# Performance work log

Hardware: AMD Instinct MI355X
Metric: run time of the kernel (lower is better)

The kernel has to match this reference:

```python
import jax, jax.numpy as jnp
import numpy as np

EMBED = 1024
FF = 4096
LN_EPS = 1e-5

def _layernorm(x, gamma, beta):
    mu = jnp.mean(x, axis=-1, keepdims=True)
    var = jnp.var(x, axis=-1, keepdims=True)
    return (x - mu) * jax.lax.rsqrt(var + LN_EPS) * gamma + beta

def setup_inputs() -> dict:
    key = jax.random.key(0)
    ks = jax.random.split(key, 16)
    s = 1.0 / np.sqrt(EMBED)
    s2 = 1.0 / np.sqrt(FF)
    return {
        "x": jax.random.normal(ks[0], (8, 2048, EMBED), dtype=jnp.float32),
        "Wq": jax.random.uniform(ks[1], (EMBED, EMBED), jnp.float32, -s, s),
        "bq": jnp.zeros((EMBED,), jnp.float32),
        "Wk": jax.random.uniform(ks[2], (EMBED, EMBED), jnp.float32, -s, s),
        "bk": jnp.zeros((EMBED,), jnp.float32),
        "Wv": jax.random.uniform(ks[3], (EMBED, EMBED), jnp.float32, -s, s),
        "bv": jnp.zeros((EMBED,), jnp.float32),
        "Wo": jax.random.uniform(ks[4], (EMBED, EMBED), jnp.float32, -s, s),
        "bo": jnp.zeros((EMBED,), jnp.float32),
        "g1": jnp.ones((EMBED,), jnp.float32),
        "b1": jnp.zeros((EMBED,), jnp.float32),
        "g2": jnp.ones((EMBED,), jnp.float32),
        "b2": jnp.zeros((EMBED,), jnp.float32),
        "W1": jax.random.uniform(ks[5], (EMBED, FF), jnp.float32, -s, s),
        "bf1": jnp.zeros((FF,), jnp.float32),
        "W2": jax.random.uniform(ks[6], (FF, EMBED), jnp.float32, -s2, s2),
        "bf2": jnp.zeros((EMBED,), jnp.float32),
    }

def reference(x, Wq, bq, Wk, bk, Wv, bv, Wo, bo, g1, b1, g2, b2, W1, bf1, W2, bf2):
    # Single-head attention (heads arg unused in original forward)
    Q = jnp.einsum('bse,ef->bsf', x, Wq) + bq
    K = jnp.einsum('bse,ef->bsf', x, Wk) + bk
    V = jnp.einsum('bse,ef->bsf', x, Wv) + bv
    scale = 1.0 / jnp.sqrt(jnp.float32(EMBED))
    scores = jnp.einsum('bqe,bke->bqk', Q, K) * scale  # [B,S,S]
    attn = jax.nn.softmax(scores, axis=-1)
    attn_out = jnp.einsum('bqk,bke->bqe', attn, V)
    attn_out = jnp.einsum('bse,ef->bsf', attn_out, Wo) + bo
    # dropout is identity in eval mode
    h = _layernorm(x + attn_out, g1, b1)
    ffn = jnp.einsum('bsf,fh->bsh', jax.nn.relu(jnp.einsum('bse,eh->bsh', h, W1) + bf1), W2) + bf2
    return _layernorm(h + ffn, g2, b2)
```

## Files before the change

kernel.cpp:

```cpp
#include <hip/hip_runtime.h>


typedef __attribute__((ext_vector_type(4))) float  f32x4;
typedef __attribute__((ext_vector_type(8))) short  s16x8;
typedef __attribute__((ext_vector_type(4))) short  s16x4;
typedef unsigned short u16;
typedef unsigned int   u32;

__device__ __forceinline__ float bf2f(short s) {
  u32 u = ((u32)(u16)s) << 16;
  float f; __builtin_memcpy(&f, &u, 4); return f;
}
__device__ __forceinline__ short f2bf(float f) {
  u32 u; __builtin_memcpy(&u, &f, 4);
  u32 r = (u + 0x7fffu + ((u >> 16) & 1u)) >> 16;
  return (short)(u16)r;
}

__device__ __forceinline__ void gload16(const void* g, void* l) {
  __builtin_amdgcn_global_load_lds(
      (const __attribute__((address_space(1))) u32*)g,
      (__attribute__((address_space(3))) u32*)l, 16, 0, 0);
}

template<int MODE>
__global__ __launch_bounds__(512, 4)
void gemm256(const u16* __restrict__ A, const u16* __restrict__ BT,
             u16* __restrict__ C,
             const float* __restrict__ bias0, const float* __restrict__ bias1,
             const float* __restrict__ bias2, const float* __restrict__ linv,
             int M, int N, int K, float scale,
             long long sA, long long sB, long long sC) {
  __shared__ u16 SMEM[24576];

  const int gx = gridDim.x, gy = gridDim.y;
  const int nwg = gx * gy * gridDim.z;
  const int orig = (blockIdx.z * gy + blockIdx.y) * gx + blockIdx.x;
  const int q = nwg >> 3, r8 = nwg & 7;
  const int xcd = orig & 7, pos = orig >> 3;
  const int wg = (xcd < r8 ? xcd * (q + 1) : r8 * (q + 1) + (xcd - r8) * q) + pos;
  const int bz = wg / (gx * gy);
  const int rem = wg % (gx * gy);
  const long long bm = (long long)(rem / gx) * 256;
  const long long bn = (long long)(rem % gx) * 128;

  const char* Ag = (const char*)(A + (long long)bz * sA);
  const char* Bg = (const char*)(BT + (long long)bz * sB);
  u16* Cb = C + (long long)bz * sC;
  const long long ldb = (long long)K * 2;

  const int tid = threadIdx.x;
  const int lane = tid & 63, wid = tid >> 6;
  const int lr = lane & 15, kg = lane >> 4;
  const int wm = wid >> 1, wn = wid & 1;
  const int NT = K >> 5;

  f32x4 acc[4][4] = {};

  const int oA0 = tid * 16, oA1 = (512 + tid) * 16, oB0 = tid * 16;
  const long long arow0 = bm + (oA0 >> 6), arow1 = bm + (oA1 >> 6);
  const long long brow0 = bn + (oB0 >> 6);
  const int akoff0 = oA0 & 63, akoff1 = oA1 & 63, bkoff0 = oB0 & 63;

#define STAGE(TT, CN) do { \
    char* sa_ = (char*)(SMEM + (CN) * 8192); \
    char* sb_ = (char*)(SMEM + 16384 + (CN) * 4096); \
    const long long kb_ = (long long)(TT) * 64; \
    gload16(Ag + arow0 * ldb + kb_ + akoff0, sa_ + oA0); \
    gload16(Ag + arow1 * ldb + kb_ + akoff1, sa_ + oA1); \
    gload16(Bg + brow0 * ldb + kb_ + bkoff0, sb_ + oB0); \
  } while (0)

  STAGE(0, 0);
  __syncthreads();

  for (int T = 0; T < NT; ++T) {
    const int c = T & 1, cn = c ^ 1;
    if (T + 1 < NT) STAGE(T + 1, cn);

    const char* pa = (const char*)(SMEM + c * 8192);
    const char* pb = (const char*)(SMEM + 16384 + c * 4096);
    s16x8 af[4], bfr[4];
#pragma unroll
    for (int mi = 0; mi < 4; ++mi)
      af[mi] = *(const s16x8*)(pa + ((wm * 64 + mi * 16 + lr) << 6) + (kg << 4));
#pragma unroll
    for (int nj = 0; nj < 4; ++nj)
      bfr[nj] = *(const s16x8*)(pb + ((wn * 64 + nj * 16 + lr) << 6) + (kg << 4));

    __builtin_amdgcn_s_setprio(1);
#pragma unroll
    for (int mi = 0; mi < 4; ++mi)
#pragma unroll
      for (int nj = 0; nj < 4; ++nj)
        acc[mi][nj] = __builtin_amdgcn_mfma_f32_16x16x32_bf16(af[mi], bfr[nj], acc[mi][nj], 0, 0, 0);
    __builtin_amdgcn_s_setprio(0);
    __syncthreads();
  }

  const long long zM = (long long)bz * M;
  u16* obase; long long ldc, bnl;
  const float* bptr = bias0;
  if (MODE == 5) {
    const int sel = (int)(bn >> 10);
    obase = C + (long long)sel * 16777216;
    ldc = 1024; bnl = bn & 1023;
    bptr = (sel == 0 ? bias0 : sel == 1 ? bias1 : bias2);
  } else { obase = Cb; ldc = N; bnl = bn; }

#pragma unroll
  for (int b = 0; b < 2; ++b) {
    if ((wm >> 1) == b) {
      const int rbase = (wm & 1) * 64;
#pragma unroll
      for (int nj = 0; nj < 4; ++nj) {
        const int col = wn * 64 + nj * 16 + lr;
        float bv = 0.f;
        if (MODE == 1 || MODE == 2 || MODE == 5) bv = bptr[bnl + col];
#pragma unroll
        for (int mi = 0; mi < 4; ++mi) {
          const int r0 = rbase + mi * 16 + kg * 4;
#pragma unroll
          for (int r = 0; r < 4; ++r) {
            float v = acc[mi][nj][r];
            if (MODE == 1 || MODE == 2 || MODE == 5) v = v * scale + bv;
            if (MODE == 2) v = fmaxf(v, 0.f);
            if (MODE == 3) v = __expf(v * scale);
            if (MODE == 4) v = v * linv[zM + bm + b * 128 + r0 + r];
            SMEM[(r0 + r) * 128 + (col ^ (kg << 4))] = (u16)f2bf(v);
          }
        }
      }
    }
    __syncthreads();
#pragma unroll
    for (int i = 0; i < 4; ++i) {
      const int o   = (i * 512 + tid) * 16;
      const int row = o >> 8;
      const int wb  = o & 255;
      const int gs  = (wb >> 4) ^ ((((row) >> 2) & 3) << 1);
      s16x8 d = *(const s16x8*)((const char*)SMEM + row * 256 + (gs << 4));
      *(s16x8*)((char*)obase + (((long long)bm + b * 128 + row) * ldc + bnl) * 2 + wb) = d;
    }
    __syncthreads();
  }
#undef STAGE
}

__global__ __launch_bounds__(256) void cast_f32_bf16(const float* __restrict__ in,
                                                     u16* __restrict__ out) {
  long long i = (long long)blockIdx.x * 256 + threadIdx.x;
  f32x4 v = ((const f32x4*)in)[i];
  s16x4 o;
#pragma unroll
  for (int j = 0; j < 4; j++) o[j] = f2bf(v[j]);
  ((s16x4*)out)[i] = o;
}

__global__ __launch_bounds__(256) void transpose_f32_bf16(const float* __restrict__ in,
                                                          u16* __restrict__ out,
                                                          int R, int C) {
  __shared__ float tile[32][33];
  const int tx = threadIdx.x, ty = threadIdx.y;
  const int r0 = blockIdx.y * 32, c0 = blockIdx.x * 32;
#pragma unroll
  for (int i = 0; i < 32; i += 8)
    tile[ty + i][tx] = in[(long long)(r0 + ty + i) * C + (c0 + tx)];
  __syncthreads();
#pragma unroll
  for (int i = 0; i < 32; i += 8)
    out[(long long)(c0 + ty + i) * R + (r0 + tx)] = (u16)f2bf(tile[tx][ty + i]);
}

__global__ __launch_bounds__(256) void transpose_bf16_bf16(const u16* __restrict__ in,
                                                           u16* __restrict__ out,
                                                           int R, int C,
                                                           long long isb, long long osb) {
  __shared__ u16 tile[32][33];
  in  += (long long)blockIdx.z * isb;
  out += (long long)blockIdx.z * osb;
  const int tx = threadIdx.x, ty = threadIdx.y;
  const int r0 = blockIdx.y * 32, c0 = blockIdx.x * 32;
#pragma unroll
  for (int i = 0; i < 32; i += 8)
    tile[ty + i][tx] = in[(long long)(r0 + ty + i) * C + (c0 + tx)];
  __syncthreads();
#pragma unroll
  for (int i = 0; i < 32; i += 8)
    out[(long long)(c0 + ty + i) * R + (r0 + tx)] = tile[tx][ty + i];
}

__global__ __launch_bounds__(256) void rowinv2048(const u16* __restrict__ P,
                                                  float* __restrict__ linv) {
  const long long row = blockIdx.x;
  const u16* p = P + row * 2048;
  const int t = threadIdx.x;
  s16x8 raw = *(const s16x8*)&p[t * 8];
  float s = 0.f;
#pragma unroll
  for (int j = 0; j < 8; j++) s += bf2f(raw[j]);
#pragma unroll
  for (int off = 32; off > 0; off >>= 1) s += __shfl_xor(s, off);
  __shared__ float red[4];
  if ((t & 63) == 0) red[t >> 6] = s;
  __syncthreads();
  if (t == 0) {
    s = (red[0] + red[1]) + (red[2] + red[3]);
    linv[row] = 1.0f / s;
  }
}

__global__ __launch_bounds__(256) void ln_add_f32bf16(const float* __restrict__ x,
                                                      const u16* __restrict__ a,
                                                      const float* __restrict__ g,
                                                      const float* __restrict__ be,
                                                      u16* __restrict__ out) {
  const long long row = blockIdx.x;
  const int t = threadIdx.x;
  f32x4 xv = ((const f32x4*)(x + row * 1024))[t];
  s16x4 av = ((const s16x4*)(a + row * 1024))[t];
  float v[4]; float sum = 0.f, ss = 0.f;
#pragma unroll
  for (int j = 0; j < 4; j++) { v[j] = xv[j] + bf2f(av[j]); sum += v[j]; ss += v[j] * v[j]; }
#pragma unroll
  for (int off = 32; off > 0; off >>= 1) { sum += __shfl_xor(sum, off); ss += __shfl_xor(ss, off); }
  __shared__ float red[8];
  if ((t & 63) == 0) { red[t >> 6] = sum; red[4 + (t >> 6)] = ss; }
  __syncthreads();
  sum = (red[0] + red[1]) + (red[2] + red[3]);
  ss  = (red[4] + red[5]) + (red[6] + red[7]);
  const float mu   = sum * (1.f / 1024.f);
  const float var  = ss * (1.f / 1024.f) - mu * mu;
  const float rstd = rsqrtf(var + 1e-5f);
  s16x4 o;
#pragma unroll
  for (int j = 0; j < 4; j++) {
    const int c = t * 4 + j;
    o[j] = f2bf((v[j] - mu) * rstd * g[c] + be[c]);
  }
  *(s16x4*)&out[row * 1024 + t * 4] = o;
}

__global__ __launch_bounds__(256) void ln_add_bf16bf16(const u16* __restrict__ h,
                                                       const u16* __restrict__ f,
                                                       const float* __restrict__ g,
                                                       const float* __restrict__ be,
                                                       float* __restrict__ out) {
  const long long row = blockIdx.x;
  const int t = threadIdx.x;
  s16x4 hv = ((const s16x4*)(h + row * 1024))[t];
  s16x4 fv = ((const s16x4*)(f + row * 1024))[t];
  float v[4]; float sum = 0.f, ss = 0.f;
#pragma unroll
  for (int j = 0; j < 4; j++) { v[j] = bf2f(hv[j]) + bf2f(fv[j]); sum += v[j]; ss += v[j] * v[j]; }
#pragma unroll
  for (int off = 32; off > 0; off >>= 1) { sum += __shfl_xor(sum, off); ss += __shfl_xor(ss, off); }
  __shared__ float red[8];
  if ((t & 63) == 0) { red[t >> 6] = sum; red[4 + (t >> 6)] = ss; }
  __syncthreads();
  sum = (red[0] + red[1]) + (red[2] + red[3]);
  ss  = (red[4] + red[5]) + (red[6] + red[7]);
  const float mu   = sum * (1.f / 1024.f);
  const float var  = ss * (1.f / 1024.f) - mu * mu;
  const float rstd = rsqrtf(var + 1e-5f);
  f32x4 o;
#pragma unroll
  for (int j = 0; j < 4; j++) {
    const int c = t * 4 + j;
    o[j] = (v[j] - mu) * rstd * g[c] + be[c];
  }
  ((f32x4*)(out + row * 1024))[t] = o;
}

extern "C" void kernel_launch(void* const* d_in, const int* in_sizes, int n_in,
                              void* d_out, int out_size, void* d_ws, size_t ws_size,
                              hipStream_t stream) {
  const float* x   = (const float*)d_in[0];
  const float* Wq  = (const float*)d_in[1];
  const float* bq  = (const float*)d_in[2];
  const float* Wk  = (const float*)d_in[3];
  const float* bk  = (const float*)d_in[4];
  const float* Wv  = (const float*)d_in[5];
  const float* bv  = (const float*)d_in[6];
  const float* Wo  = (const float*)d_in[7];
  const float* bo  = (const float*)d_in[8];
  const float* g1  = (const float*)d_in[9];
  const float* b1  = (const float*)d_in[10];
  const float* g2  = (const float*)d_in[11];
  const float* b2  = (const float*)d_in[12];
  const float* W1  = (const float*)d_in[13];
  const float* bf1 = (const float*)d_in[14];
  const float* W2  = (const float*)d_in[15];
  const float* bf2 = (const float*)d_in[16];
  float* out = (float*)d_out;

  char* ws = (char*)d_ws;
  u16* wsWQT = (u16*)(ws + 0);
  u16* wsWKT = (u16*)(ws + 2097152);
  u16* wsWVT = (u16*)(ws + 4194304);
  u16* wsWOT = (u16*)(ws + 6291456);
  u16* wsW1T = (u16*)(ws + 8388608);
  u16* wsW2T = (u16*)(ws + 16777216);
  u16* wsXB  = (u16*)(ws + 25165824);
  u16* wsQ   = (u16*)(ws + 58720256);
  u16* wsK   = (u16*)(ws + 92274688);
  u16* wsV   = (u16*)(ws + 125829120);
  u16* wsVT  = (u16*)(ws + 159383552);
  u16* wsS   = (u16*)(ws + 192937984);
  u16* wsAO  = wsXB;
  u16* wsAO2 = wsQ;
  u16* wsH   = wsK;
  u16* wsHID = wsV;
  u16* wsFFN = wsXB;
  float* wsLINV = (float*)wsQ;

  const dim3 tb(32, 8, 1);
  const float inv_sqrt_e = 0.03125f;
  const float* nf = nullptr;

  cast_f32_bf16<<<16384, 256, 0, stream>>>(x, wsXB);

  transpose_f32_bf16<<<dim3(32, 32, 1),  tb, 0, stream>>>(Wq, wsWQT, 1024, 1024);
  transpose_f32_bf16<<<dim3(32, 32, 1),  tb, 0, stream>>>(Wk, wsWKT, 1024, 1024);
  transpose_f32_bf16<<<dim3(32, 32, 1),  tb, 0, stream>>>(Wv, wsWVT, 1024, 1024);
  transpose_f32_bf16<<<dim3(32, 32, 1),  tb, 0, stream>>>(Wo, wsWOT, 1024, 1024);
  transpose_f32_bf16<<<dim3(128, 32, 1), tb, 0, stream>>>(W1, wsW1T, 1024, 4096);
  transpose_f32_bf16<<<dim3(32, 128, 1), tb, 0, stream>>>(W2, wsW2T, 4096, 1024);

  gemm256<5><<<dim3(24, 64, 1), 512, 0, stream>>>(wsXB, wsWQT, wsQ, bq, bk, bv, nf,
                                                  16384, 3072, 1024, 1.f, 0, 0, 0);

  transpose_bf16_bf16<<<dim3(32, 64, 8), tb, 0, stream>>>(wsV, wsVT, 2048, 1024, 2048LL * 1024, 1024LL * 2048);

  gemm256<3><<<dim3(16, 8, 8), 512, 0, stream>>>(wsQ, wsK, wsS, nf, nf, nf, nf,
                                                 2048, 2048, 1024, inv_sqrt_e,
                                                 2048LL * 1024, 2048LL * 1024, 2048LL * 2048);
  rowinv2048<<<16384, 256, 0, stream>>>(wsS, wsLINV);

  gemm256<4><<<dim3(8, 8, 8), 512, 0, stream>>>(wsS, wsVT, wsAO, nf, nf, nf, wsLINV,
                                                2048, 1024, 2048, 1.f,
                                                2048LL * 2048, 1024LL * 2048, 2048LL * 1024);
  gemm256<1><<<dim3(8, 64, 1), 512, 0, stream>>>(wsAO, wsWOT, wsAO2, bo, nf, nf, nf,
                                                 16384, 1024, 1024, 1.f, 0, 0, 0);

  ln_add_f32bf16<<<16384, 256, 0, stream>>>(x, wsAO2, g1, b1, wsH);

  gemm256<2><<<dim3(32, 64, 1), 512, 0, stream>>>(wsH, wsW1T, wsHID, bf1, nf, nf, nf,
                                                  16384, 4096, 1024, 1.f, 0, 0, 0);

  gemm256<1><<<dim3(8, 64, 1), 512, 0, stream>>>(wsHID, wsW2T, wsFFN, bf2, nf, nf, nf,
                                                 16384, 1024, 4096, 1.f, 0, 0, 0);

  ln_add_bf16bf16<<<16384, 256, 0, stream>>>(wsH, wsFFN, g2, b2, out);

  (void)in_sizes; (void)n_in; (void)out_size; (void)ws_size;
}
```

Before: 689.2 us.

## Triple-buffer GEMM LDS staging with swizzled layout and vmcnt-based waits

Moves the GEMM main loop from double to triple buffering in LDS, issuing loads two tiles ahead. Each iteration now waits with an explicit vmcnt count and one barrier instead of a full syncthreads at the end. It also XOR-swizzles the 16-byte chunk within each 64-byte row, applied on the global source side so the direct-to-LDS copies land swizzled and fragment reads avoid bank conflicts. The cost is larger LDS use per block (72KB), which may limit how many blocks fit per CU, plus reliance on hand-counted vmcnt values.

```diff
diff --git a/kernel.cpp b/kernel.cpp
--- a/kernel.cpp
+++ b/kernel.cpp
@@ -31,7 +31,7 @@
              const float* __restrict__ bias2, const float* __restrict__ linv,
              int M, int N, int K, float scale,
              long long sA, long long sB, long long sC) {
-  __shared__ u16 SMEM[24576];
+  __shared__ u16 SMEM[36864];
 
   const int gx = gridDim.x, gy = gridDim.y;
   const int nwg = gx * gy * gridDim.z;
@@ -58,35 +58,47 @@
   f32x4 acc[4][4] = {};
 
   const int oA0 = tid * 16, oA1 = (512 + tid) * 16, oB0 = tid * 16;
-  const long long arow0 = bm + (oA0 >> 6), arow1 = bm + (oA1 >> 6);
-  const long long brow0 = bn + (oB0 >> 6);
-  const int akoff0 = oA0 & 63, akoff1 = oA1 & 63, bkoff0 = oB0 & 63;
-
-#define STAGE(TT, CN) do { \
-    char* sa_ = (char*)(SMEM + (CN) * 8192); \
-    char* sb_ = (char*)(SMEM + 16384 + (CN) * 4096); \
+  const int rA0 = oA0 >> 6, rA1 = oA1 >> 6, rB0 = oB0 >> 6;
+  const long long arow0 = bm + rA0, arow1 = bm + rA1;
+  const long long brow0 = bn + rB0;
+  const int asrc0 = (oA0 & 63) ^ (((rA0 >> 1) & 3) << 4);
+  const int asrc1 = (oA1 & 63) ^ (((rA1 >> 1) & 3) << 4);
+  const int bsrc0 = (oB0 & 63) ^ (((rB0 >> 1) & 3) << 4);
+
+#define STAGE(TT, CC) do { \
+    char* sa_ = (char*)(SMEM + (CC) * 8192); \
+    char* sb_ = (char*)(SMEM + 24576 + (CC) * 4096); \
     const long long kb_ = (long long)(TT) * 64; \
-    gload16(Ag + arow0 * ldb + kb_ + akoff0, sa_ + oA0); \
-    gload16(Ag + arow1 * ldb + kb_ + akoff1, sa_ + oA1); \
-    gload16(Bg + brow0 * ldb + kb_ + bkoff0, sb_ + oB0); \
+    gload16(Ag + arow0 * ldb + kb_ + asrc0, sa_ + oA0); \
+    gload16(Ag + arow1 * ldb + kb_ + asrc1, sa_ + oA1); \
+    gload16(Bg + brow0 * ldb + kb_ + bsrc0, sb_ + oB0); \
   } while (0)
 
   STAGE(0, 0);
-  __syncthreads();
-
+  STAGE(1, 1);
+
+  int c = 0;
   for (int T = 0; T < NT; ++T) {
-    const int c = T & 1, cn = c ^ 1;
-    if (T + 1 < NT) STAGE(T + 1, cn);
+    if (T + 1 < NT) { asm volatile("s_waitcnt vmcnt(3)"); }
+    else            { asm volatile("s_waitcnt vmcnt(0)"); }
+    __builtin_amdgcn_s_barrier();
+    __builtin_amdgcn_sched_barrier(0);
+
+    if (T + 2 < NT) STAGE(T + 2, (T + 2) % 3);
 
     const char* pa = (const char*)(SMEM + c * 8192);
-    const char* pb = (const char*)(SMEM + 16384 + c * 4096);
+    const char* pb = (const char*)(SMEM + 24576 + c * 4096);
     s16x8 af[4], bfr[4];
 #pragma unroll
-    for (int mi = 0; mi < 4; ++mi)
-      af[mi] = *(const s16x8*)(pa + ((wm * 64 + mi * 16 + lr) << 6) + (kg << 4));
-#pragma unroll
-    for (int nj = 0; nj < 4; ++nj)
-      bfr[nj] = *(const s16x8*)(pb + ((wn * 64 + nj * 16 + lr) << 6) + (kg << 4));
+    for (int mi = 0; mi < 4; ++mi) {
+      const int row_ = wm * 64 + mi * 16 + lr;
+      af[mi] = *(const s16x8*)(pa + (row_ << 6) + ((kg ^ ((row_ >> 1) & 3)) << 4));
+    }
+#pragma unroll
+    for (int nj = 0; nj < 4; ++nj) {
+      const int row_ = wn * 64 + nj * 16 + lr;
+      bfr[nj] = *(const s16x8*)(pb + (row_ << 6) + ((kg ^ ((row_ >> 1) & 3)) << 4));
+    }
 
     __builtin_amdgcn_s_setprio(1);
 #pragma unroll
@@ -95,8 +107,10 @@
       for (int nj = 0; nj < 4; ++nj)
         acc[mi][nj] = __builtin_amdgcn_mfma_f32_16x16x32_bf16(af[mi], bfr[nj], acc[mi][nj], 0, 0, 0);
     __builtin_amdgcn_s_setprio(0);
-    __syncthreads();
-  }
+
+    c = (c + 1) % 3;
+  }
+  __syncthreads();
 
   const long long zM = (long long)bz * M;
   u16* obase; long long ldc, bnl;
```

Result: no change. 687.5 us (-0.2%).
